# Kernel optimization log

Measured on AMD Instinct MI355X. Metric: run time of the kernel, lower is better.

The kernel has to match this reference:

```python
import jax, jax.numpy as jnp
import numpy as np

DIM_HEAD = 128
HEADS = 16
SCALE = DIM_HEAD ** -0.5


def rotate_half(t):
    # '... (j d) -> ... j d' with j=2: split into first/second halves
    x1, x2 = jnp.split(t, 2, axis=-1)
    return jnp.concatenate((-x2, x1), axis=-1)


def apply_rope(pos, t):
    # pos: [n, d]; t: [..., n, d]
    return t * jnp.cos(pos) + rotate_half(t) * jnp.sin(pos)


def setup_inputs() -> dict:
    key = jax.random.key(0)
    k0, k1, k2, k3 = jax.random.split(key, 4)
    b, n, dim = 2, 2048, 2048
    inner = HEADS * DIM_HEAD
    return {
        "x": jax.random.normal(k0, (b, n, dim), jnp.float32),
        "Wq": jax.random.normal(k1, (dim, inner), jnp.float32) * 0.02,
        "Wkv": jax.random.normal(k2, (dim, 2 * DIM_HEAD), jnp.float32) * 0.02,
        "Wout": jax.random.normal(k3, (inner, dim), jnp.float32) * 0.02,
    }


def reference(x, Wq, Wkv, Wout):
    b, n, dim = x.shape
    # projections from the UN-normalized x (norm in original is dead code)
    q = x @ Wq                               # [b, n, h*d]
    kv = x @ Wkv                             # [b, n, 2d]
    k, v = jnp.split(kv, 2, axis=-1)         # each [b, n, d] (multi-query)
    q = q.reshape(b, n, HEADS, DIM_HEAD).transpose(0, 2, 1, 3)  # [b,h,n,d]

    # rotary positions
    inv_freq = 1.0 / (10000.0 ** (jnp.arange(0, DIM_HEAD, 2, dtype=jnp.float32) / DIM_HEAD))
    freqs = jnp.arange(n, dtype=jnp.float32)[:, None] * inv_freq[None, :]
    pos = jnp.concatenate((freqs, freqs), axis=-1)  # [n, d]

    q = apply_rope(pos, q) * SCALE
    k = apply_rope(pos, k)

    sim = jnp.einsum('bhid,bjd->bhij', q, k)  # [b,h,n,n]
    causal_mask = jnp.triu(jnp.ones((n, n), dtype=bool), 1)
    neg = -jnp.finfo(sim.dtype).max
    sim = jnp.where(causal_mask, neg, sim)
    sim = sim - jax.lax.stop_gradient(jnp.max(sim, axis=-1, keepdims=True))
    attn = jax.nn.softmax(sim, axis=-1)

    out = jnp.einsum('bhij,bjd->bhid', attn, v)          # [b,h,n,d]
    out = out.transpose(0, 2, 1, 3).reshape(b, n, HEADS * DIM_HEAD)
    return out @ Wout
```

## Files before the change

### kernel.cpp

```cpp
#include <hip/hip_runtime.h>
#include <hip/hip_bf16.h>
#include <cstddef>
#include <cstdint>

#define BATCH 2
#define SEQ   2048
#define DIM   2048
#define HEADS 16
#define DHEAD 128
#define INNER (HEADS * DHEAD)
#define MROWS (BATCH * SEQ)
#define ATT_SCALE 0.08838834764831845f
#define QK_SCALE (0.08838834764831845f * 1.4426950408889634f)
#define NEG_LOG2_10000_DIV64 (-13.287712379549449f / 64.0f)
#define M_HAT 12.0f

typedef __attribute__((ext_vector_type(8))) short short8;
typedef __attribute__((ext_vector_type(4))) short short4v;
typedef __attribute__((ext_vector_type(4))) float f32x4;

static __device__ __forceinline__ short f2bf(float x) {
    uint32_t u = __float_as_uint(x);
    uint32_t r = (u + 0x7fffu + ((u >> 16) & 1u)) >> 16;
    return (short)r;
}
static __device__ __forceinline__ float bf2f(short s) {
    return __uint_as_float(((uint32_t)(uint16_t)s) << 16);
}
static __device__ __forceinline__ short2 f2bf2(float a, float b) {
    __hip_bfloat162 h = __float22bfloat162_rn(make_float2(a, b));
    return *reinterpret_cast<short2*>(&h);
}

static __device__ __forceinline__ void glds16(const short* g, short* l) {
    __builtin_amdgcn_global_load_lds(
        (const __attribute__((address_space(1))) unsigned int*)g,
        (__attribute__((address_space(3))) unsigned int*)l, 16, 0, 0);
}

static __device__ __forceinline__ int swz_row(int r) {
    return (r & 3) | ((r >> 1) & 4);
}

static __device__ __forceinline__ void tcast_body(const float* __restrict__ W,
                                                  short* __restrict__ Wt,
                                                  int R, int C, int bx, int by,
                                                  int tid, float (*tile)[65]) {
    const int c0 = bx * 64, r0 = by * 64;
#pragma unroll
    for (int t = 0; t < 4; ++t) {
        int idx = tid + t * 256;
        int row = idx >> 4, col4 = idx & 15;
        float4 v = *(const float4*)&W[(size_t)(r0 + row) * C + c0 + col4 * 4];
        tile[row][col4 * 4 + 0] = v.x;
        tile[row][col4 * 4 + 1] = v.y;
        tile[row][col4 * 4 + 2] = v.z;
        tile[row][col4 * 4 + 3] = v.w;
    }
    __syncthreads();
#pragma unroll
    for (int t = 0; t < 4; ++t) {
        int idx = tid + t * 256;
        int r = idx >> 4, c4 = idx & 15;
        short2 s01 = f2bf2(tile[c4 * 4 + 0][r], tile[c4 * 4 + 1][r]);
        short2 s23 = f2bf2(tile[c4 * 4 + 2][r], tile[c4 * 4 + 3][r]);
        short4v s = {s01.x, s01.y, s23.x, s23.y};
        *(short4v*)&Wt[(size_t)(c0 + r) * R + r0 + c4 * 4] = s;
    }
}

__global__ __launch_bounds__(256) void prep(const float* __restrict__ x,
                                            short* __restrict__ xb,
                                            const float* __restrict__ Wq,
                                            short* __restrict__ Wt,
                                            const float* __restrict__ Wkv,
                                            short* __restrict__ Wkvt,
                                            const float* __restrict__ Wout,
                                            short* __restrict__ WtO,
                                            float2* __restrict__ lut) {
    __shared__ float tile[64][65];
    const int bid = blockIdx.x;
    const int tid = threadIdx.x;
    if (bid < 8192) {
        int i = bid * 256 + tid;
        float4 v = ((const float4*)x)[i];
        short2 s01 = f2bf2(v.x, v.y), s23 = f2bf2(v.z, v.w);
        short4v s = {s01.x, s01.y, s23.x, s23.y};
        ((short4v*)xb)[i] = s;
    } else if (bid < 9216) {
        int t = bid - 8192;
        tcast_body(Wq, Wt, DIM, INNER, t & 31, t >> 5, tid, tile);
    } else if (bid < 9344) {
        int t = bid - 9216;
        tcast_body(Wkv, Wkvt, DIM, 256, t & 3, t >> 2, tid, tile);
    } else if (bid < 10368) {
        int t = bid - 9344;
        tcast_body(Wout, WtO, INNER, DIM, t & 31, t >> 5, tid, tile);
    } else {
        int t = (bid - 10368) * 256 + tid;
        int j = t >> 11;
        int pos = t & (SEQ - 1);
        float ang = (float)pos * exp2f((float)j * NEG_LOG2_10000_DIV64);
        lut[(size_t)j * SEQ + pos] = make_float2(cosf(ang), sinf(ang));
    }
}

static __device__ __forceinline__ void wait_vmcnt8() {
    asm volatile("s_waitcnt vmcnt(8)" ::: "memory");
}
static __device__ __forceinline__ void wait_vmcnt0() {
    asm volatile("s_waitcnt vmcnt(0)" ::: "memory");
}

__global__ __launch_bounds__(256) void gemm_qkv(const short* __restrict__ A,
                                                const short* __restrict__ Bt,
                                                short* __restrict__ qout,
                                                short* __restrict__ kbout,
                                                short* __restrict__ vtout,
                                                const float2* __restrict__ lut) {
    __shared__ __align__(16) short sA[2][128 * 64];
    __shared__ __align__(16) short sB[2][128 * 64];
    const int K = DIM;

    const int tid = threadIdx.x;
    const int w = tid >> 6, lane = tid & 63;
    const int ln = lane & 15, qr = lane >> 4;
    const int bm = blockIdx.y * 128, bn = blockIdx.x * 128;
    const int wm = (w >> 1) * 64;
    const int wn2 = (w & 1) * 32;

    const f32x4 zero4 = {0.f, 0.f, 0.f, 0.f};
    f32x4 acc[4][4];
#pragma unroll
    for (int mt = 0; mt < 4; ++mt)
#pragma unroll
        for (int nt = 0; nt < 4; ++nt) acc[mt][nt] = zero4;

    int offG[4], ldsO[4];
#pragma unroll
    for (int t = 0; t < 4; ++t) {
        int row = w * 32 + t * 8 + (lane >> 3);
        int c = (lane & 7) ^ (row & 7);
        offG[t] = row * K + c * 8;
        ldsO[t] = (w * 32 + t * 8) * 64;
    }
    const short* pA = A + (size_t)bm * K;
    const short* pB = Bt + (size_t)bn * K;

#pragma unroll
    for (int t = 0; t < 4; ++t) glds16(pA + offG[t], &sA[0][ldsO[t]]);
#pragma unroll
    for (int t = 0; t < 4; ++t) glds16(pB + offG[t], &sB[0][ldsO[t]]);
#pragma unroll
    for (int t = 0; t < 4; ++t) glds16(pA + 64 + offG[t], &sA[1][ldsO[t]]);
#pragma unroll
    for (int t = 0; t < 4; ++t) glds16(pB + 64 + offG[t], &sB[1][ldsO[t]]);

    const int NT = K / 64;
    for (int kt = 0; kt < NT; ++kt) {
        const int cur = kt & 1;
        if (kt < NT - 2) wait_vmcnt8();
        else             wait_vmcnt0();
        __builtin_amdgcn_s_barrier();

#pragma unroll
        for (int ks = 0; ks < 2; ++ks) {
            short8 af[4], bfr[4];
#pragma unroll
            for (int mt = 0; mt < 4; ++mt) {
                const int row = wm + mt * 16 + ln;
                af[mt] = *(const short8*)&sA[cur][row * 64 +
                    (((ks << 2) + qr) ^ (row & 7)) * 8];
            }
#pragma unroll
            for (int nt = 0; nt < 4; ++nt) {
                const int colr = wn2 + ((nt & 1) << 4) + ((nt >> 1) << 6) + ln;
                bfr[nt] = *(const short8*)&sB[cur][colr * 64 +
                    (((ks << 2) + qr) ^ (colr & 7)) * 8];
            }
            __builtin_amdgcn_s_setprio(1);
#pragma unroll
            for (int mt = 0; mt < 4; ++mt)
#pragma unroll
                for (int nt = 0; nt < 4; ++nt)
                    acc[mt][nt] = __builtin_amdgcn_mfma_f32_16x16x32_bf16(
                        af[mt], bfr[nt], acc[mt][nt], 0, 0, 0);
            __builtin_amdgcn_s_setprio(0);
        }

        __builtin_amdgcn_s_barrier();
        if (kt + 2 < NT) {
            const int ko = (kt + 2) * 64;
#pragma unroll
            for (int t = 0; t < 4; ++t)
                glds16(pA + ko + offG[t], &sA[cur][ldsO[t]]);
#pragma unroll
            for (int t = 0; t < 4; ++t)
                glds16(pB + ko + offG[t], &sB[cur][ldsO[t]]);
        }
    }

    if (bn <= INNER) {
        const float scale = (bn < INNER) ? QK_SCALE : 1.0f;
#pragma unroll
        for (int mt = 0; mt < 4; ++mt) {
#pragma unroll
            for (int nt = 0; nt < 2; ++nt) {
                const int d0 = wn2 + nt * 16 + ln;
                const int row0 = wm + mt * 16 + qr * 4;
                const int pos0 = (bm + row0) & (SEQ - 1);
                const float4* lp = (const float4*)&lut[(size_t)d0 * SEQ + pos0];
                const float4 c01 = lp[0];
                const float4 c23 = lp[1];
                const float cx[4] = {c01.x, c01.z, c23.x, c23.z};
                const float cy[4] = {c01.y, c01.w, c23.y, c23.w};
#pragma unroll
                for (int r = 0; r < 4; ++r) {
                    const float a = acc[mt][nt][r];
                    const float b = acc[mt][nt + 2][r];
                    const float lo = (a * cx[r] - b * cy[r]) * scale;
                    const float hi = (b * cx[r] + a * cy[r]) * scale;
                    const int row = row0 + r;
                    if (bn < INNER) {
                        short* q0 = qout + (size_t)(bm + row) * INNER + bn + d0;
                        q0[0] = f2bf(lo);
                        q0[64] = f2bf(hi);
                    } else {
                        short* k0p = kbout + (size_t)(bm + row) * DHEAD + d0;
                        k0p[0] = f2bf(lo);
                        k0p[64] = f2bf(hi);
                    }
                }
            }
        }
    } else {
        const int gb = bm >> 11;
        const int pos_base = bm & (SEQ - 1);
#pragma unroll
        for (int mt = 0; mt < 4; ++mt) {
#pragma unroll
            for (int nt = 0; nt < 4; ++nt) {
                const int cn = wn2 + ((nt & 1) << 4) + ((nt >> 1) << 6) + ln;
                const int pos0 = pos_base + wm + mt * 16 + qr * 4;
                short2 s01 = f2bf2(acc[mt][nt][0], acc[mt][nt][1]);
                short2 s23 = f2bf2(acc[mt][nt][2], acc[mt][nt][3]);
                short4v sv = {s01.x, s01.y, s23.x, s23.y};
                *(short4v*)&vtout[((size_t)gb * DHEAD + cn) * SEQ + pos0] = sv;
            }
        }
    }
}

__global__ __launch_bounds__(256) void gemm_bt(const short* __restrict__ A,
                                               const short* __restrict__ Bt,
                                               float* __restrict__ C,
                                               int M, int N, int K) {
    __shared__ __align__(16) short sA[2][128 * 64];
    __shared__ __align__(16) short sB[2][128 * 64];

    const int tid = threadIdx.x;
    const int w = tid >> 6, lane = tid & 63;
    const int ln = lane & 15, qr = lane >> 4;
    const int bm = blockIdx.y * 128, bn = blockIdx.x * 128;
    const int wm = (w >> 1) * 64, wn = (w & 1) * 64;

    const f32x4 zero4 = {0.f, 0.f, 0.f, 0.f};
    f32x4 acc[4][4];
#pragma unroll
    for (int mt = 0; mt < 4; ++mt)
#pragma unroll
        for (int nt = 0; nt < 4; ++nt) acc[mt][nt] = zero4;

    int offG[4], ldsO[4];
#pragma unroll
    for (int t = 0; t < 4; ++t) {
        int row = w * 32 + t * 8 + (lane >> 3);
        int c = (lane & 7) ^ (row & 7);
        offG[t] = row * K + c * 8;
        ldsO[t] = (w * 32 + t * 8) * 64;
    }
    const short* pA = A + (size_t)bm * K;
    const short* pB = Bt + (size_t)bn * K;

#pragma unroll
    for (int t = 0; t < 4; ++t) glds16(pA + offG[t], &sA[0][ldsO[t]]);
#pragma unroll
    for (int t = 0; t < 4; ++t) glds16(pB + offG[t], &sB[0][ldsO[t]]);
#pragma unroll
    for (int t = 0; t < 4; ++t) glds16(pA + 64 + offG[t], &sA[1][ldsO[t]]);
#pragma unroll
    for (int t = 0; t < 4; ++t) glds16(pB + 64 + offG[t], &sB[1][ldsO[t]]);

    const int NT = K / 64;
    for (int kt = 0; kt < NT; ++kt) {
        const int cur = kt & 1;
        if (kt < NT - 2) wait_vmcnt8();
        else             wait_vmcnt0();
        __builtin_amdgcn_s_barrier();

#pragma unroll
        for (int ks = 0; ks < 2; ++ks) {
            short8 af[4], bfr[4];
#pragma unroll
            for (int mt = 0; mt < 4; ++mt) {
                const int row = wm + mt * 16 + ln;
                af[mt] = *(const short8*)&sA[cur][row * 64 +
                    (((ks << 2) + qr) ^ (row & 7)) * 8];
            }
#pragma unroll
            for (int nt = 0; nt < 4; ++nt) {
                const int colr = wn + nt * 16 + ln;
                bfr[nt] = *(const short8*)&sB[cur][colr * 64 +
                    (((ks << 2) + qr) ^ (colr & 7)) * 8];
            }
            __builtin_amdgcn_s_setprio(1);
#pragma unroll
            for (int mt = 0; mt < 4; ++mt)
#pragma unroll
                for (int nt = 0; nt < 4; ++nt)
                    acc[mt][nt] = __builtin_amdgcn_mfma_f32_16x16x32_bf16(
                        af[mt], bfr[nt], acc[mt][nt], 0, 0, 0);
            __builtin_amdgcn_s_setprio(0);
        }

        __builtin_amdgcn_s_barrier();
        if (kt + 2 < NT) {
            const int ko = (kt + 2) * 64;
#pragma unroll
            for (int t = 0; t < 4; ++t)
                glds16(pA + ko + offG[t], &sA[cur][ldsO[t]]);
#pragma unroll
            for (int t = 0; t < 4; ++t)
                glds16(pB + ko + offG[t], &sB[cur][ldsO[t]]);
        }
    }

#pragma unroll
    for (int mt = 0; mt < 4; ++mt)
#pragma unroll
        for (int nt = 0; nt < 4; ++nt)
#pragma unroll
            for (int r = 0; r < 4; ++r)
                C[(size_t)(bm + wm + mt * 16 + qr * 4 + r) * N +
                  bn + wn + nt * 16 + ln] = acc[mt][nt][r];
}

__global__ __launch_bounds__(512) void attn_mfma(const short* __restrict__ qb,
                                                 const short* __restrict__ kb,
                                                 const short* __restrict__ vt,
                                                 short* __restrict__ o) {
    __shared__ __align__(16) short sK[2][2][64 * 128];
    __shared__ __align__(16) short sV[2][2][128 * 64];
    __shared__ float lred[4][2][64];

    const int bid = blockIdx.x;
    const int p = bid & 7;
    const int bh = bid >> 3;
    const int h = bh & (HEADS - 1);
    const int b = bh >> 4;

    const int tid = threadIdx.x;
    const int w = tid >> 6;
    const int g = w >> 2;
    const int wg = w & 3;
    const int lane = tid & 63;
    const int ln = lane & 15;
    const int qr = lane >> 4;

    const short* kbase = kb + (size_t)b * SEQ * DHEAD;
    const short* vbase = vt + (size_t)b * DHEAD * SEQ;

    int offK[4], offV[4], ldsK[4], ldsV[4];
#pragma unroll
    for (int t = 0; t < 4; ++t) {
        int rk = wg * 16 + t * 4 + (lane >> 4);
        int ck = (lane & 15) ^ swz_row(rk);
        offK[t] = rk * DHEAD + ck * 8;
        ldsK[t] = (wg * 16 + t * 4) * 128;
        int rv = wg * 32 + t * 8 + (lane >> 3);
        int cv = (lane & 7) ^ swz_row(rv);
        offV[t] = rv * SEQ + cv * 8;
        ldsV[t] = (wg * 32 + t * 8) * 64;
    }

    for (int ph = 0; ph < 2; ++ph) {
        const int it = ph ? p : (15 - p);
        const int i0 = it * 128;
        const int njt = 2 * it + 2;
        const int half = njt >> 1;
        const int igmax = i0 + wg * 32 + 31;

        short8 qf[2][4];
#pragma unroll
        for (int qs = 0; qs < 2; ++qs) {
            const size_t qrow =
                ((size_t)(b * SEQ + i0 + wg * 32 + qs * 16 + ln)) * INNER + h * DHEAD;
#pragma unroll
            for (int ks = 0; ks < 4; ++ks)
                qf[qs][ks] = *(const short8*)&qb[qrow + ks * 32 + qr * 8];
        }

        const f32x4 zero4 = {0.f, 0.f, 0.f, 0.f};
        const f32x4 mhat4 = {-M_HAT, -M_HAT, -M_HAT, -M_HAT};
        f32x4 oa[2][8];
#pragma unroll
        for (int qs = 0; qs < 2; ++qs)
#pragma unroll
            for (int dt = 0; dt < 8; ++dt) oa[qs][dt] = zero4;
        float lsum[2] = {0.f, 0.f};

        __syncthreads();
        {
            const size_t kof = (size_t)g * 64 * DHEAD;
            const size_t vof = (size_t)g * 64;
#pragma unroll
            for (int t = 0; t < 4; ++t)
                glds16(kbase + kof + offK[t], &sK[g][0][ldsK[t]]);
#pragma unroll
            for (int t = 0; t < 4; ++t)
                glds16(vbase + vof + offV[t], &sV[g][0][ldsV[t]]);
        }

        for (int k = 0; k < half; ++k) {
            const int cur = k & 1;
            const int jt = 2 * k + g;
            __syncthreads();
            if (k + 1 < half) {
                const size_t kof = (size_t)(jt + 2) * 64 * DHEAD;
                const size_t vof = (size_t)(jt + 2) * 64;
#pragma unroll
                for (int t = 0; t < 4; ++t)
                    glds16(kbase + kof + offK[t], &sK[g][cur ^ 1][ldsK[t]]);
#pragma unroll
                for (int t = 0; t < 4; ++t)
                    glds16(vbase + vof + offV[t], &sV[g][cur ^ 1][ldsV[t]]);
            }
            if (jt * 64 > igmax) continue;

            f32x4 sacc[2][4];
#pragma unroll
            for (int qs = 0; qs < 2; ++qs)
#pragma unroll
                for (int nt = 0; nt < 4; ++nt) sacc[qs][nt] = mhat4;
            __builtin_amdgcn_s_setprio(1);
#pragma unroll
            for (int nt = 0; nt < 4; ++nt) {
                const int row = ((nt >> 1) << 5) + ((ln >> 2) << 3) +
                                ((nt & 1) << 2) + (ln & 3);
                const int sw = ln & 7;
#pragma unroll
                for (int ks = 0; ks < 4; ++ks) {
                    short8 kf = *(const short8*)&sK[g][cur][row * 128 + ((4 * ks + qr) ^ sw) * 8];
                    sacc[0][nt] = __builtin_amdgcn_mfma_f32_16x16x32_bf16(
                        kf, qf[0][ks], sacc[0][nt], 0, 0, 0);
                    sacc[1][nt] = __builtin_amdgcn_mfma_f32_16x16x32_bf16(
                        kf, qf[1][ks], sacc[1][nt], 0, 0, 0);
                }
            }
            __builtin_amdgcn_s_setprio(0);

            short8 pb[2][2];
#pragma unroll
            for (int qs = 0; qs < 2; ++qs) {
                const int ig = i0 + wg * 32 + qs * 16 + ln;
                if (jt * 64 + 63 > ig) {
#pragma unroll
                    for (int nt = 0; nt < 4; ++nt)
#pragma unroll
                        for (int r = 0; r < 4; ++r) {
                            int jg = jt * 64 + ((nt >> 1) << 5) + qr * 8 +
                                     ((nt & 1) << 2) + r;
                            if (jg > ig) sacc[qs][nt][r] = -3.0e38f;
                        }
                }
                float rs = 0.f;
                float pv[4][4];
#pragma unroll
                for (int nt = 0; nt < 4; ++nt)
#pragma unroll
                    for (int r = 0; r < 4; ++r) {
                        float e = exp2f(sacc[qs][nt][r]);
                        pv[nt][r] = e;
                        rs += e;
                    }
                rs += __shfl_xor(rs, 16);
                rs += __shfl_xor(rs, 32);
                lsum[qs] += rs;
#pragma unroll
                for (int kb2 = 0; kb2 < 2; ++kb2) {
                    short2* pp = (short2*)&pb[qs][kb2];
                    pp[0] = f2bf2(pv[2 * kb2][0], pv[2 * kb2][1]);
                    pp[1] = f2bf2(pv[2 * kb2][2], pv[2 * kb2][3]);
                    pp[2] = f2bf2(pv[2 * kb2 + 1][0], pv[2 * kb2 + 1][1]);
                    pp[3] = f2bf2(pv[2 * kb2 + 1][2], pv[2 * kb2 + 1][3]);
                }
            }

            __builtin_amdgcn_s_setprio(1);
#pragma unroll
            for (int kb2 = 0; kb2 < 2; ++kb2) {
#pragma unroll
                for (int dt = 0; dt < 8; ++dt) {
                    const int row = dt * 16 + ln;
                    short8 vf = *(const short8*)&sV[g][cur][row * 64 +
                        ((4 * kb2 + qr) ^ swz_row(row)) * 8];
                    oa[0][dt] = __builtin_amdgcn_mfma_f32_16x16x32_bf16(
                        vf, pb[0][kb2], oa[0][dt], 0, 0, 0);
                    oa[1][dt] = __builtin_amdgcn_mfma_f32_16x16x32_bf16(
                        vf, pb[1][kb2], oa[1][dt], 0, 0, 0);
                }
            }
            __builtin_amdgcn_s_setprio(0);
        }

        f32x4* cb = (f32x4*)&sK[1][0][0];
        __syncthreads();
        if (g == 1) {
#pragma unroll
            for (int dt = 0; dt < 8; ++dt)
                cb[dt * 256 + wg * 64 + lane] = oa[0][dt];
            lred[wg][0][lane] = lsum[0];
            lred[wg][1][lane] = lsum[1];
        }
        __syncthreads();
        if (g == 0) {
#pragma unroll
            for (int dt = 0; dt < 8; ++dt)
                oa[0][dt] += cb[dt * 256 + wg * 64 + lane];
            lsum[0] += lred[wg][0][lane];
            lsum[1] += lred[wg][1][lane];
        }
        __syncthreads();
        if (g == 1) {
#pragma unroll
            for (int dt = 0; dt < 8; ++dt)
                cb[dt * 256 + wg * 64 + lane] = oa[1][dt];
        }
        __syncthreads();
        if (g == 0) {
#pragma unroll
            for (int dt = 0; dt < 8; ++dt)
                oa[1][dt] += cb[dt * 256 + wg * 64 + lane];
#pragma unroll
            for (int qs = 0; qs < 2; ++qs) {
                const float invl = 1.f / lsum[qs];
                short* orow = o + ((size_t)(b * SEQ + i0 + wg * 32 + qs * 16 + ln)) * INNER +
                              h * DHEAD;
#pragma unroll
                for (int dt = 0; dt < 8; ++dt) {
                    short2 s01 = f2bf2(oa[qs][dt][0] * invl, oa[qs][dt][1] * invl);
                    short2 s23 = f2bf2(oa[qs][dt][2] * invl, oa[qs][dt][3] * invl);
                    short4v sv = {s01.x, s01.y, s23.x, s23.y};
                    *(short4v*)&orow[dt * 16 + qr * 4] = sv;
                }
            }
        }
    }
}

extern "C" void kernel_launch(void* const* d_in, const int* in_sizes, int n_in,
                              void* d_out, int out_size, void* d_ws, size_t ws_size,
                              hipStream_t stream) {
    const float* x    = (const float*)d_in[0];
    const float* Wq   = (const float*)d_in[1];
    const float* Wkv  = (const float*)d_in[2];
    const float* Wout = (const float*)d_in[3];
    float* out = (float*)d_out;

    short* xb    = (short*)d_ws;
    short* Wt    = xb + (size_t)MROWS * DIM;
    short* Wkvt  = Wt + (size_t)DIM * INNER;
    short* WtO   = Wkvt + (size_t)256 * DIM;
    short* qb    = WtO + (size_t)DIM * INNER;
    short* kb    = qb + (size_t)MROWS * INNER;
    short* vt    = kb + (size_t)MROWS * DHEAD;
    float2* lut  = (float2*)(vt + (size_t)BATCH * DHEAD * SEQ);
    short* ob    = xb;

    prep<<<10880, 256, 0, stream>>>(x, xb, Wq, Wt, Wkv, Wkvt, Wout, WtO, lut);
    gemm_qkv<<<dim3(18, 32), 256, 0, stream>>>(xb, Wt, qb, kb, vt, lut);
    attn_mfma<<<256, 512, 0, stream>>>(qb, kb, vt, ob);
    gemm_bt<<<dim3(16, 32), 256, 0, stream>>>(ob, WtO, out, MROWS, DIM, INNER);
}
```

Baseline: 285.3 us.

## Use four-stage 32-wide K pipeline in projection GEMMs

Both bf16 GEMM kernels switch from a two-buffer 64-wide K tile to a four-buffer 32-wide K tile, keeping the same LDS footprint. Prefetch is issued four stages ahead, with graduated vmcnt waits and an XOR swizzle adjusted for the narrower rows. The aim is to hide more global-load latency. In exchange there are twice as many barriers per K and fewer MFMAs between synchronisations.

```diff
diff --git a/kernel.cpp b/kernel.cpp
--- a/kernel.cpp
+++ b/kernel.cpp
@@ -40,6 +40,19 @@
 
 static __device__ __forceinline__ int swz_row(int r) {
     return (r & 3) | ((r >> 1) & 4);
+}
+
+static __device__ __forceinline__ void wait_vmcnt12() {
+    asm volatile("s_waitcnt vmcnt(12)" ::: "memory");
+}
+static __device__ __forceinline__ void wait_vmcnt8() {
+    asm volatile("s_waitcnt vmcnt(8)" ::: "memory");
+}
+static __device__ __forceinline__ void wait_vmcnt4() {
+    asm volatile("s_waitcnt vmcnt(4)" ::: "memory");
+}
+static __device__ __forceinline__ void wait_vmcnt0() {
+    asm volatile("s_waitcnt vmcnt(0)" ::: "memory");
 }
 
 static __device__ __forceinline__ void tcast_body(const float* __restrict__ W,
@@ -105,21 +118,14 @@
     }
 }
 
-static __device__ __forceinline__ void wait_vmcnt8() {
-    asm volatile("s_waitcnt vmcnt(8)" ::: "memory");
-}
-static __device__ __forceinline__ void wait_vmcnt0() {
-    asm volatile("s_waitcnt vmcnt(0)" ::: "memory");
-}
-
 __global__ __launch_bounds__(256) void gemm_qkv(const short* __restrict__ A,
                                                 const short* __restrict__ Bt,
                                                 short* __restrict__ qout,
                                                 short* __restrict__ kbout,
                                                 short* __restrict__ vtout,
                                                 const float2* __restrict__ lut) {
-    __shared__ __align__(16) short sA[2][128 * 64];
-    __shared__ __align__(16) short sB[2][128 * 64];
+    __shared__ __align__(16) short sA[4][128 * 32];
+    __shared__ __align__(16) short sB[4][128 * 32];
     const int K = DIM;
 
     const int tid = threadIdx.x;
@@ -136,66 +142,62 @@
 #pragma unroll
         for (int nt = 0; nt < 4; ++nt) acc[mt][nt] = zero4;
 
-    int offG[4], ldsO[4];
-#pragma unroll
-    for (int t = 0; t < 4; ++t) {
-        int row = w * 32 + t * 8 + (lane >> 3);
-        int c = (lane & 7) ^ (row & 7);
+    int offG[2], ldsO[2];
+#pragma unroll
+    for (int t = 0; t < 2; ++t) {
+        int row = w * 32 + t * 16 + (lane >> 2);
+        int c = (lane & 3) ^ (row & 3);
         offG[t] = row * K + c * 8;
-        ldsO[t] = (w * 32 + t * 8) * 64;
+        ldsO[t] = (w * 32 + t * 16) * 32;
     }
     const short* pA = A + (size_t)bm * K;
     const short* pB = Bt + (size_t)bn * K;
 
 #pragma unroll
-    for (int t = 0; t < 4; ++t) glds16(pA + offG[t], &sA[0][ldsO[t]]);
-#pragma unroll
-    for (int t = 0; t < 4; ++t) glds16(pB + offG[t], &sB[0][ldsO[t]]);
-#pragma unroll
-    for (int t = 0; t < 4; ++t) glds16(pA + 64 + offG[t], &sA[1][ldsO[t]]);
-#pragma unroll
-    for (int t = 0; t < 4; ++t) glds16(pB + 64 + offG[t], &sB[1][ldsO[t]]);
-
-    const int NT = K / 64;
+    for (int p = 0; p < 4; ++p) {
+#pragma unroll
+        for (int t = 0; t < 2; ++t) glds16(pA + p * 32 + offG[t], &sA[p][ldsO[t]]);
+#pragma unroll
+        for (int t = 0; t < 2; ++t) glds16(pB + p * 32 + offG[t], &sB[p][ldsO[t]]);
+    }
+
+    const int NT = K / 32;
     for (int kt = 0; kt < NT; ++kt) {
-        const int cur = kt & 1;
-        if (kt < NT - 2) wait_vmcnt8();
-        else             wait_vmcnt0();
+        const int cur = kt & 3;
+        if (kt < NT - 3)       wait_vmcnt12();
+        else if (kt == NT - 3) wait_vmcnt8();
+        else if (kt == NT - 2) wait_vmcnt4();
+        else                   wait_vmcnt0();
         __builtin_amdgcn_s_barrier();
 
-#pragma unroll
-        for (int ks = 0; ks < 2; ++ks) {
-            short8 af[4], bfr[4];
-#pragma unroll
-            for (int mt = 0; mt < 4; ++mt) {
-                const int row = wm + mt * 16 + ln;
-                af[mt] = *(const short8*)&sA[cur][row * 64 +
-                    (((ks << 2) + qr) ^ (row & 7)) * 8];
-            }
-#pragma unroll
-            for (int nt = 0; nt < 4; ++nt) {
-                const int colr = wn2 + ((nt & 1) << 4) + ((nt >> 1) << 6) + ln;
-                bfr[nt] = *(const short8*)&sB[cur][colr * 64 +
-                    (((ks << 2) + qr) ^ (colr & 7)) * 8];
-            }
-            __builtin_amdgcn_s_setprio(1);
-#pragma unroll
-            for (int mt = 0; mt < 4; ++mt)
-#pragma unroll
-                for (int nt = 0; nt < 4; ++nt)
-                    acc[mt][nt] = __builtin_amdgcn_mfma_f32_16x16x32_bf16(
-                        af[mt], bfr[nt], acc[mt][nt], 0, 0, 0);
-            __builtin_amdgcn_s_setprio(0);
-        }
+        short8 af[4], bfr[4];
+#pragma unroll
+        for (int mt = 0; mt < 4; ++mt) {
+            const int row = wm + mt * 16 + ln;
+            af[mt] = *(const short8*)&sA[cur][row * 32 + (qr ^ (row & 3)) * 8];
+        }
+#pragma unroll
+        for (int nt = 0; nt < 4; ++nt) {
+            const int colr = wn2 + ((nt & 1) << 4) + ((nt >> 1) << 6) + ln;
+            bfr[nt] = *(const short8*)&sB[cur][colr * 32 + (qr ^ (colr & 3)) * 8];
+        }
+        __builtin_amdgcn_s_setprio(1);
+#pragma unroll
+        for (int mt = 0; mt < 4; ++mt)
+#pragma unroll
+            for (int nt = 0; nt < 4; ++nt)
+                acc[mt][nt] = __builtin_amdgcn_mfma_f32_16x16x32_bf16(
+                    af[mt], bfr[nt], acc[mt][nt], 0, 0, 0);
+        __builtin_amdgcn_s_setprio(0);
 
         __builtin_amdgcn_s_barrier();
-        if (kt + 2 < NT) {
-            const int ko = (kt + 2) * 64;
-#pragma unroll
-            for (int t = 0; t < 4; ++t)
+        if (kt + 4 < NT) {
+            const int ko = (kt + 4) * 32;
+#pragma unroll
+            for (int t = 0; t < 2; ++t)
                 glds16(pA + ko + offG[t], &sA[cur][ldsO[t]]);
 #pragma unroll
-            for (int t = 0; t < 4; ++t)
+            for (int t = 0; t < 2; ++t)
                 glds16(pB + ko + offG[t], &sB[cur][ldsO[t]]);
         }
     }
@@ -255,8 +257,8 @@
                                                const short* __restrict__ Bt,
                                                float* __restrict__ C,
                                                int M, int N, int K) {
-    __shared__ __align__(16) short sA[2][128 * 64];
-    __shared__ __align__(16) short sB[2][128 * 64];
+    __shared__ __align__(16) short sA[4][128 * 32];
+    __shared__ __align__(16) short sB[4][128 * 32];
 
     const int tid = threadIdx.x;
     const int w = tid >> 6, lane = tid & 63;
@@ -271,66 +273,62 @@
 #pragma unroll
         for (int nt = 0; nt < 4; ++nt) acc[mt][nt] = zero4;
 
-    int offG[4], ldsO[4];
-#pragma unroll
-    for (int t = 0; t < 4; ++t) {
-        int row = w * 32 + t * 8 + (lane >> 3);
-        int c = (lane & 7) ^ (row & 7);
+    int offG[2], ldsO[2];
+#pragma unroll
+    for (int t = 0; t < 2; ++t) {
+        int row = w * 32 + t * 16 + (lane >> 2);
+        int c = (lane & 3) ^ (row & 3);
         offG[t] = row * K + c * 8;
-        ldsO[t] = (w * 32 + t * 8) * 64;
+        ldsO[t] = (w * 32 + t * 16) * 32;
     }
     const short* pA = A + (size_t)bm * K;
     const short* pB = Bt + (size_t)bn * K;
 
 #pragma unroll
-    for (int t = 0; t < 4; ++t) glds16(pA + offG[t], &sA[0][ldsO[t]]);
-#pragma unroll
-    for (int t = 0; t < 4; ++t) glds16(pB + offG[t], &sB[0][ldsO[t]]);
-#pragma unroll
-    for (int t = 0; t < 4; ++t) glds16(pA + 64 + offG[t], &sA[1][ldsO[t]]);
-#pragma unroll
-    for (int t = 0; t < 4; ++t) glds16(pB + 64 + offG[t], &sB[1][ldsO[t]]);
-
-    const int NT = K / 64;
+    for (int p = 0; p < 4; ++p) {
+#pragma unroll
+        for (int t = 0; t < 2; ++t) glds16(pA + p * 32 + offG[t], &sA[p][ldsO[t]]);
+#pragma unroll
+        for (int t = 0; t < 2; ++t) glds16(pB + p * 32 + offG[t], &sB[p][ldsO[t]]);
+    }
+
+    const int NT = K / 32;
     for (int kt = 0; kt < NT; ++kt) {
-        const int cur = kt & 1;
-        if (kt < NT - 2) wait_vmcnt8();
-        else             wait_vmcnt0();
+        const int cur = kt & 3;
+        if (kt < NT - 3)       wait_vmcnt12();
+        else if (kt == NT - 3) wait_vmcnt8();
+        else if (kt == NT - 2) wait_vmcnt4();
+        else                   wait_vmcnt0();
         __builtin_amdgcn_s_barrier();
 
-#pragma unroll
-        for (int ks = 0; ks < 2; ++ks) {
-            short8 af[4], bfr[4];
-#pragma unroll
-            for (int mt = 0; mt < 4; ++mt) {
-                const int row = wm + mt * 16 + ln;
-                af[mt] = *(const short8*)&sA[cur][row * 64 +
-                    (((ks << 2) + qr) ^ (row & 7)) * 8];
-            }
-#pragma unroll
-            for (int nt = 0; nt < 4; ++nt) {
-                const int colr = wn + nt * 16 + ln;
-                bfr[nt] = *(const short8*)&sB[cur][colr * 64 +
-                    (((ks << 2) + qr) ^ (colr & 7)) * 8];
-            }
-            __builtin_amdgcn_s_setprio(1);
-#pragma unroll
-            for (int mt = 0; mt < 4; ++mt)
-#pragma unroll
-                for (int nt = 0; nt < 4; ++nt)
-                    acc[mt][nt] = __builtin_amdgcn_mfma_f32_16x16x32_bf16(
-                        af[mt], bfr[nt], acc[mt][nt], 0, 0, 0);
-            __builtin_amdgcn_s_setprio(0);
-        }
+        short8 af[4], bfr[4];
+#pragma unroll
+        for (int mt = 0; mt < 4; ++mt) {
+            const int row = wm + mt * 16 + ln;
+            af[mt] = *(const short8*)&sA[cur][row * 32 + (qr ^ (row & 3)) * 8];
+        }
+#pragma unroll
+        for (int nt = 0; nt < 4; ++nt) {
+            const int colr = wn + nt * 16 + ln;
+            bfr[nt] = *(const short8*)&sB[cur][colr * 32 + (qr ^ (colr & 3)) * 8];
+        }
+        __builtin_amdgcn_s_setprio(1);
+#pragma unroll
+        for (int mt = 0; mt < 4; ++mt)
+#pragma unroll
+            for (int nt = 0; nt < 4; ++nt)
+                acc[mt][nt] = __builtin_amdgcn_mfma_f32_16x16x32_bf16(
+                    af[mt], bfr[nt], acc[mt][nt], 0, 0, 0);
+        __builtin_amdgcn_s_setprio(0);
 
         __builtin_amdgcn_s_barrier();
-        if (kt + 2 < NT) {
-            const int ko = (kt + 2) * 64;
-#pragma unroll
-            for (int t = 0; t < 4; ++t)
+        if (kt + 4 < NT) {
+            const int ko = (kt + 4) * 32;
+#pragma unroll
+            for (int t = 0; t < 2; ++t)
                 glds16(pA + ko + offG[t], &sA[cur][ldsO[t]]);
 #pragma unroll
-            for (int t = 0; t < 4; ++t)
+            for (int t = 0; t < 2; ++t)
                 glds16(pB + ko + offG[t], &sB[cur][ldsO[t]]);
         }
     }
```

Result: slower. 304.4 us (+6.7%).

## Enlarge GEMM tiles to 128x256 with 8 waves and triple-buffered LDS

Applied to the files above, without the earlier changes.

Both the QKV projection GEMM and the output GEMM now use 512-thread blocks computing 128x256 tiles, which halves the grid. LDS staging moves from double to triple buffering, with the next-next tile issued right after the barrier, so one barrier per k-step is dropped. The larger tile increases reuse of the A operand, and the deeper pipeline is meant to hide global load latency. In exchange, LDS use per block rises to 144 KB, which likely allows only one block per CU, and with a smaller grid of 288 or 256 blocks some CUs may sit idle.

```diff
diff --git a/kernel.cpp b/kernel.cpp
--- a/kernel.cpp
+++ b/kernel.cpp
@@ -40,6 +40,13 @@
 
 static __device__ __forceinline__ int swz_row(int r) {
     return (r & 3) | ((r >> 1) & 4);
+}
+
+static __device__ __forceinline__ void wait_vmcnt6() {
+    asm volatile("s_waitcnt vmcnt(6)" ::: "memory");
+}
+static __device__ __forceinline__ void wait_vmcnt0() {
+    asm volatile("s_waitcnt vmcnt(0)" ::: "memory");
 }
 
 static __device__ __forceinline__ void tcast_body(const float* __restrict__ W,
@@ -105,110 +112,112 @@
     }
 }
 
-static __device__ __forceinline__ void wait_vmcnt8() {
-    asm volatile("s_waitcnt vmcnt(8)" ::: "memory");
-}
-static __device__ __forceinline__ void wait_vmcnt0() {
-    asm volatile("s_waitcnt vmcnt(0)" ::: "memory");
-}
-
-__global__ __launch_bounds__(256) void gemm_qkv(const short* __restrict__ A,
+__global__ __launch_bounds__(512) void gemm_qkv(const short* __restrict__ A,
                                                 const short* __restrict__ Bt,
                                                 short* __restrict__ qout,
                                                 short* __restrict__ kbout,
                                                 short* __restrict__ vtout,
                                                 const float2* __restrict__ lut) {
-    __shared__ __align__(16) short sA[2][128 * 64];
-    __shared__ __align__(16) short sB[2][128 * 64];
+    __shared__ __align__(16) short sA[3][128 * 64];
+    __shared__ __align__(16) short sB[3][256 * 64];
     const int K = DIM;
 
     const int tid = threadIdx.x;
     const int w = tid >> 6, lane = tid & 63;
     const int ln = lane & 15, qr = lane >> 4;
-    const int bm = blockIdx.y * 128, bn = blockIdx.x * 128;
-    const int wm = (w >> 1) * 64;
-    const int wn2 = (w & 1) * 32;
+    const int wmi = w >> 2, wni = w & 3;
+    const int bx = blockIdx.x;
+    const int bm = blockIdx.y * 128;
 
     const f32x4 zero4 = {0.f, 0.f, 0.f, 0.f};
     f32x4 acc[4][4];
 #pragma unroll
-    for (int mt = 0; mt < 4; ++mt)
-#pragma unroll
-        for (int nt = 0; nt < 4; ++nt) acc[mt][nt] = zero4;
-
-    int offG[4], ldsO[4];
-#pragma unroll
-    for (int t = 0; t < 4; ++t) {
-        int row = w * 32 + t * 8 + (lane >> 3);
-        int c = (lane & 7) ^ (row & 7);
-        offG[t] = row * K + c * 8;
-        ldsO[t] = (w * 32 + t * 8) * 64;
+    for (int mf = 0; mf < 4; ++mf)
+#pragma unroll
+        for (int nf = 0; nf < 4; ++nf) acc[mf][nf] = zero4;
+
+    int offA[2], ldsA[2], offB[4], ldsB[4];
+#pragma unroll
+    for (int j = 0; j < 2; ++j) {
+        int ra = (j * 8 + w) * 8 + (lane >> 3);
+        int ca = (lane & 7) ^ (ra & 7);
+        offA[j] = ra * K + ca * 8;
+        ldsA[j] = (j * 8 + w) * 8 * 64;
+    }
+#pragma unroll
+    for (int j = 0; j < 4; ++j) {
+        int rb = (j * 8 + w) * 8 + (lane >> 3);
+        int cb2 = (lane & 7) ^ (rb & 7);
+        offB[j] = rb * K + cb2 * 8;
+        ldsB[j] = (j * 8 + w) * 8 * 64;
     }
     const short* pA = A + (size_t)bm * K;
-    const short* pB = Bt + (size_t)bn * K;
-
-#pragma unroll
-    for (int t = 0; t < 4; ++t) glds16(pA + offG[t], &sA[0][ldsO[t]]);
-#pragma unroll
-    for (int t = 0; t < 4; ++t) glds16(pB + offG[t], &sB[0][ldsO[t]]);
-#pragma unroll
-    for (int t = 0; t < 4; ++t) glds16(pA + 64 + offG[t], &sA[1][ldsO[t]]);
-#pragma unroll
-    for (int t = 0; t < 4; ++t) glds16(pB + 64 + offG[t], &sB[1][ldsO[t]]);
+    const short* pB = Bt + (size_t)bx * 256 * K;
+
+#pragma unroll
+    for (int j = 0; j < 2; ++j) glds16(pA + offA[j], &sA[0][ldsA[j]]);
+#pragma unroll
+    for (int j = 0; j < 4; ++j) glds16(pB + offB[j], &sB[0][ldsB[j]]);
+#pragma unroll
+    for (int j = 0; j < 2; ++j) glds16(pA + 64 + offA[j], &sA[1][ldsA[j]]);
+#pragma unroll
+    for (int j = 0; j < 4; ++j) glds16(pB + 64 + offB[j], &sB[1][ldsB[j]]);
 
     const int NT = K / 64;
+    int buf = 0, sbuf = 2;
     for (int kt = 0; kt < NT; ++kt) {
-        const int cur = kt & 1;
-        if (kt < NT - 2) wait_vmcnt8();
+        if (kt < NT - 1) wait_vmcnt6();
         else             wait_vmcnt0();
         __builtin_amdgcn_s_barrier();
 
+        if (kt + 2 < NT) {
+            const int ko = (kt + 2) * 64;
+#pragma unroll
+            for (int j = 0; j < 2; ++j) glds16(pA + ko + offA[j], &sA[sbuf][ldsA[j]]);
+#pragma unroll
+            for (int j = 0; j < 4; ++j) glds16(pB + ko + offB[j], &sB[sbuf][ldsB[j]]);
+        }
+
 #pragma unroll
         for (int ks = 0; ks < 2; ++ks) {
             short8 af[4], bfr[4];
 #pragma unroll
-            for (int mt = 0; mt < 4; ++mt) {
-                const int row = wm + mt * 16 + ln;
-                af[mt] = *(const short8*)&sA[cur][row * 64 +
+            for (int mf = 0; mf < 4; ++mf) {
+                const int row = wmi * 64 + mf * 16 + ln;
+                af[mf] = *(const short8*)&sA[buf][row * 64 +
                     (((ks << 2) + qr) ^ (row & 7)) * 8];
             }
 #pragma unroll
-            for (int nt = 0; nt < 4; ++nt) {
-                const int colr = wn2 + ((nt & 1) << 4) + ((nt >> 1) << 6) + ln;
-                bfr[nt] = *(const short8*)&sB[cur][colr * 64 +
+            for (int nf = 0; nf < 4; ++nf) {
+                const int colr = (wni >> 1) * 128 + (wni & 1) * 32 +
+                                 (nf & 1) * 16 + (nf >> 1) * 64 + ln;
+                bfr[nf] = *(const short8*)&sB[buf][colr * 64 +
                     (((ks << 2) + qr) ^ (colr & 7)) * 8];
             }
             __builtin_amdgcn_s_setprio(1);
 #pragma unroll
-            for (int mt = 0; mt < 4; ++mt)
-#pragma unroll
-                for (int nt = 0; nt < 4; ++nt)
-                    acc[mt][nt] = __builtin_amdgcn_mfma_f32_16x16x32_bf16(
-                        af[mt], bfr[nt], acc[mt][nt], 0, 0, 0);
+            for (int mf = 0; mf < 4; ++mf)
+#pragma unroll
+                for (int nf = 0; nf < 4; ++nf)
+                    acc[mf][nf] = __builtin_amdgcn_mfma_f32_16x16x32_bf16(
+                        af[mf], bfr[nf], acc[mf][nf], 0, 0, 0);
             __builtin_amdgcn_s_setprio(0);
         }
-
-        __builtin_amdgcn_s_barrier();
-        if (kt + 2 < NT) {
-            const int ko = (kt + 2) * 64;
-#pragma unroll
-            for (int t = 0; t < 4; ++t)
-                glds16(pA + ko + offG[t], &sA[cur][ldsO[t]]);
-#pragma unroll
-            for (int t = 0; t < 4; ++t)
-                glds16(pB + ko + offG[t], &sB[cur][ldsO[t]]);
-        }
-    }
-
-    if (bn <= INNER) {
-        const float scale = (bn < INNER) ? QK_SCALE : 1.0f;
-#pragma unroll
-        for (int mt = 0; mt < 4; ++mt) {
-#pragma unroll
-            for (int nt = 0; nt < 2; ++nt) {
-                const int d0 = wn2 + nt * 16 + ln;
-                const int row0 = wm + mt * 16 + qr * 4;
-                const int pos0 = (bm + row0) & (SEQ - 1);
+        buf = (buf == 2) ? 0 : buf + 1;
+        sbuf = (sbuf == 2) ? 0 : sbuf + 1;
+    }
+
+    const int rbase = bm + wmi * 64;
+    if (bx < 8 || wni < 2) {
+        const float scale = (bx < 8) ? QK_SCALE : 1.0f;
+        const int hs = wni >> 1;
+#pragma unroll
+        for (int mf = 0; mf < 4; ++mf) {
+#pragma unroll
+            for (int nf = 0; nf < 2; ++nf) {
+                const int d0 = (wni & 1) * 32 + nf * 16 + ln;
+                const int row0 = rbase + mf * 16 + qr * 4;
+                const int pos0 = row0 & (SEQ - 1);
                 const float4* lp = (const float4*)&lut[(size_t)d0 * SEQ + pos0];
                 const float4 c01 = lp[0];
                 const float4 c23 = lp[1];
@@ -216,17 +225,17 @@
                 const float cy[4] = {c01.y, c01.w, c23.y, c23.w};
 #pragma unroll
                 for (int r = 0; r < 4; ++r) {
-                    const float a = acc[mt][nt][r];
-                    const float b = acc[mt][nt + 2][r];
+                    const float a = acc[mf][nf][r];
+                    const float b = acc[mf][nf + 2][r];
                     const float lo = (a * cx[r] - b * cy[r]) * scale;
                     const float hi = (b * cx[r] + a * cy[r]) * scale;
-                    const int row = row0 + r;
-                    if (bn < INNER) {
-                        short* q0 = qout + (size_t)(bm + row) * INNER + bn + d0;
+                    if (bx < 8) {
+                        short* q0 = qout + (size_t)(row0 + r) * INNER +
+                                    bx * 256 + hs * 128 + d0;
                         q0[0] = f2bf(lo);
                         q0[64] = f2bf(hi);
                     } else {
-                        short* k0p = kbout + (size_t)(bm + row) * DHEAD + d0;
+                        short* k0p = kbout + (size_t)(row0 + r) * DHEAD + d0;
                         k0p[0] = f2bf(lo);
                         k0p[64] = f2bf(hi);
                     }
@@ -235,114 +244,121 @@
         }
     } else {
         const int gb = bm >> 11;
-        const int pos_base = bm & (SEQ - 1);
-#pragma unroll
-        for (int mt = 0; mt < 4; ++mt) {
-#pragma unroll
-            for (int nt = 0; nt < 4; ++nt) {
-                const int cn = wn2 + ((nt & 1) << 4) + ((nt >> 1) << 6) + ln;
-                const int pos0 = pos_base + wm + mt * 16 + qr * 4;
-                short2 s01 = f2bf2(acc[mt][nt][0], acc[mt][nt][1]);
-                short2 s23 = f2bf2(acc[mt][nt][2], acc[mt][nt][3]);
+        const int posb = (bm & (SEQ - 1)) + wmi * 64;
+#pragma unroll
+        for (int mf = 0; mf < 4; ++mf) {
+#pragma unroll
+            for (int nf = 0; nf < 4; ++nf) {
+                const int cv = (wni & 1) * 32 + (nf & 1) * 16 + (nf >> 1) * 64 + ln;
+                const int pos0 = posb + mf * 16 + qr * 4;
+                short2 s01 = f2bf2(acc[mf][nf][0], acc[mf][nf][1]);
+                short2 s23 = f2bf2(acc[mf][nf][2], acc[mf][nf][3]);
                 short4v sv = {s01.x, s01.y, s23.x, s23.y};
-                *(short4v*)&vtout[((size_t)gb * DHEAD + cn) * SEQ + pos0] = sv;
-            }
-        }
-    }
-}
-
-__global__ __launch_bounds__(256) void gemm_bt(const short* __restrict__ A,
+                *(short4v*)&vtout[((size_t)gb * DHEAD + cv) * SEQ + pos0] = sv;
+            }
+        }
+    }
+}
+
+__global__ __launch_bounds__(512) void gemm_bt(const short* __restrict__ A,
                                                const short* __restrict__ Bt,
                                                float* __restrict__ C,
                                                int M, int N, int K) {
-    __shared__ __align__(16) short sA[2][128 * 64];
-    __shared__ __align__(16) short sB[2][128 * 64];
+    __shared__ __align__(16) short sA[3][128 * 64];
+    __shared__ __align__(16) short sB[3][256 * 64];
 
     const int tid = threadIdx.x;
     const int w = tid >> 6, lane = tid & 63;
     const int ln = lane & 15, qr = lane >> 4;
-    const int bm = blockIdx.y * 128, bn = blockIdx.x * 128;
-    const int wm = (w >> 1) * 64, wn = (w & 1) * 64;
+    const int wmi = w >> 2, wni = w & 3;
+    const int bn = blockIdx.x * 256;
+    const int bm = blockIdx.y * 128;
 
     const f32x4 zero4 = {0.f, 0.f, 0.f, 0.f};
     f32x4 acc[4][4];
 #pragma unroll
-    for (int mt = 0; mt < 4; ++mt)
-#pragma unroll
-        for (int nt = 0; nt < 4; ++nt) acc[mt][nt] = zero4;
-
-    int offG[4], ldsO[4];
-#pragma unroll
-    for (int t = 0; t < 4; ++t) {
-        int row = w * 32 + t * 8 + (lane >> 3);
-        int c = (lane & 7) ^ (row & 7);
-        offG[t] = row * K + c * 8;
-        ldsO[t] = (w * 32 + t * 8) * 64;
+    for (int mf = 0; mf < 4; ++mf)
+#pragma unroll
+        for (int nf = 0; nf < 4; ++nf) acc[mf][nf] = zero4;
+
+    int offA[2], ldsA[2], offB[4], ldsB[4];
+#pragma unroll
+    for (int j = 0; j < 2; ++j) {
+        int ra = (j * 8 + w) * 8 + (lane >> 3);
+        int ca = (lane & 7) ^ (ra & 7);
+        offA[j] = ra * K + ca * 8;
+        ldsA[j] = (j * 8 + w) * 8 * 64;
+    }
+#pragma unroll
+    for (int j = 0; j < 4; ++j) {
+        int rb = (j * 8 + w) * 8 + (lane >> 3);
+        int cb2 = (lane & 7) ^ (rb & 7);
+        offB[j] = rb * K + cb2 * 8;
+        ldsB[j] = (j * 8 + w) * 8 * 64;
     }
     const short* pA = A + (size_t)bm * K;
     const short* pB = Bt + (size_t)bn * K;
 
 #pragma unroll
-    for (int t = 0; t < 4; ++t) glds16(pA + offG[t], &sA[0][ldsO[t]]);
-#pragma unroll
-    for (int t = 0; t < 4; ++t) glds16(pB + offG[t], &sB[0][ldsO[t]]);
-#pragma unroll
-    for (int t = 0; t < 4; ++t) glds16(pA + 64 + offG[t], &sA[1][ldsO[t]]);
-#pragma unroll
-    for (int t = 0; t < 4; ++t) glds16(pB + 64 + offG[t], &sB[1][ldsO[t]]);
+    for (int j = 0; j < 2; ++j) glds16(pA + offA[j], &sA[0][ldsA[j]]);
+#pragma unroll
+    for (int j = 0; j < 4; ++j) glds16(pB + offB[j], &sB[0][ldsB[j]]);
+#pragma unroll
+    for (int j = 0; j < 2; ++j) glds16(pA + 64 + offA[j], &sA[1][ldsA[j]]);
+#pragma unroll
+    for (int j = 0; j < 4; ++j) glds16(pB + 64 + offB[j], &sB[1][ldsB[j]]);
 
     const int NT = K / 64;
+    int buf = 0, sbuf = 2;
     for (int kt = 0; kt < NT; ++kt) {
-        const int cur = kt & 1;
-        if (kt < NT - 2) wait_vmcnt8();
+        if (kt < NT - 1) wait_vmcnt6();
         else             wait_vmcnt0();
         __builtin_amdgcn_s_barrier();
 
+        if (kt + 2 < NT) {
+            const int ko = (kt + 2) * 64;
+#pragma unroll
+            for (int j = 0; j < 2; ++j) glds16(pA + ko + offA[j], &sA[sbuf][ldsA[j]]);
+#pragma unroll
+            for (int j = 0; j < 4; ++j) glds16(pB + ko + offB[j], &sB[sbuf][ldsB[j]]);
+        }
+
 #pragma unroll
         for (int ks = 0; ks < 2; ++ks) {
             short8 af[4], bfr[4];
 #pragma unroll
-            for (int mt = 0; mt < 4; ++mt) {
-                const int row = wm + mt * 16 + ln;
-                af[mt] = *(const short8*)&sA[cur][row * 64 +
+            for (int mf = 0; mf < 4; ++mf) {
+                const int row = wmi * 64 + mf * 16 + ln;
+                af[mf] = *(const short8*)&sA[buf][row * 64 +
                     (((ks << 2) + qr) ^ (row & 7)) * 8];
             }
 #pragma unroll
-            for (int nt = 0; nt < 4; ++nt) {
-                const int colr = wn + nt * 16 + ln;
-                bfr[nt] = *(const short8*)&sB[cur][colr * 64 +
+            for (int nf = 0; nf < 4; ++nf) {
+                const int colr = wni * 64 + nf * 16 + ln;
+                bfr[nf] = *(const short8*)&sB[buf][colr * 64 +
                     (((ks << 2) + qr) ^ (colr & 7)) * 8];
             }
             __builtin_amdgcn_s_setprio(1);
 #pragma unroll
-            for (int mt = 0; mt < 4; ++mt)
-#pragma unroll
-                for (int nt = 0; nt < 4; ++nt)
-                    acc[mt][nt] = __builtin_amdgcn_mfma_f32_16x16x32_bf16(
-                        af[mt], bfr[nt], acc[mt][nt], 0, 0, 0);
+            for (int mf = 0; mf < 4; ++mf)
+#pragma unroll
+                for (int nf = 0; nf < 4; ++nf)
+                    acc[mf][nf] = __builtin_amdgcn_mfma_f32_16x16x32_bf16(
+                        af[mf], bfr[nf], acc[mf][nf], 0, 0, 0);
             __builtin_amdgcn_s_setprio(0);
         }
-
-        __builtin_amdgcn_s_barrier();
-        if (kt + 2 < NT) {
-            const int ko = (kt + 2) * 64;
-#pragma unroll
-            for (int t = 0; t < 4; ++t)
-                glds16(pA + ko + offG[t], &sA[cur][ldsO[t]]);
-#pragma unroll
-            for (int t = 0; t < 4; ++t)
-                glds16(pB + ko + offG[t], &sB[cur][ldsO[t]]);
-        }
-    }
-
-#pragma unroll
-    for (int mt = 0; mt < 4; ++mt)
-#pragma unroll
-        for (int nt = 0; nt < 4; ++nt)
+        buf = (buf == 2) ? 0 : buf + 1;
+        sbuf = (sbuf == 2) ? 0 : sbuf + 1;
+    }
+
+#pragma unroll
+    for (int mf = 0; mf < 4; ++mf)
+#pragma unroll
+        for (int nf = 0; nf < 4; ++nf)
 #pragma unroll
             for (int r = 0; r < 4; ++r)
-                C[(size_t)(bm + wm + mt * 16 + qr * 4 + r) * N +
-                  bn + wn + nt * 16 + ln] = acc[mt][nt][r];
+                C[(size_t)(bm + wmi * 64 + mf * 16 + qr * 4 + r) * N +
+                  bn + wni * 64 + nf * 16 + ln] = acc[mf][nf][r];
 }
 
 __global__ __launch_bounds__(512) void attn_mfma(const short* __restrict__ qb,
@@ -578,7 +594,7 @@
     short* ob    = xb;
 
     prep<<<10880, 256, 0, stream>>>(x, xb, Wq, Wt, Wkv, Wkvt, Wout, WtO, lut);
-    gemm_qkv<<<dim3(18, 32), 256, 0, stream>>>(xb, Wt, qb, kb, vt, lut);
+    gemm_qkv<<<dim3(9, 32), 512, 0, stream>>>(xb, Wt, qb, kb, vt, lut);
     attn_mfma<<<256, 512, 0, stream>>>(qb, kb, vt, ob);
-    gemm_bt<<<dim3(16, 32), 256, 0, stream>>>(ob, WtO, out, MROWS, DIM, INNER);
-}
+    gemm_bt<<<dim3(8, 32), 512, 0, stream>>>(ob, WtO, out, MROWS, DIM, INNER);
+}
```

After: 314.1 us. 10.1% more time.
